# Kernel tuning notes

Measured on AMD Instinct MI355X. Metric: run time of the kernel, lower is better.

The kernel has to match this reference:

```python
import jax, jax.numpy as jnp
import numpy as np
import math

N_HEADS = 12
ROPE_DIM = 64
BASE = 10000.0


def _rope_tables(seq_len, dim):
    inv_freq = 1.0 / (BASE ** (jnp.arange(0, dim, 2, dtype=jnp.float32) / dim))
    t = jnp.arange(seq_len, dtype=jnp.float32)
    freqs = jnp.outer(t, inv_freq)                      # [S, dim/2]
    emb = jnp.concatenate([freqs, freqs], axis=-1)      # [S, dim]
    # broadcast shape [1, S, 1, dim]
    return jnp.cos(emb)[None, :, None, :], jnp.sin(emb)[None, :, None, :]


def _rotate_half(x):
    x1, x2 = jnp.split(x, 2, axis=-1)
    return jnp.concatenate([-x2, x1], axis=-1)


def setup_inputs() -> dict:
    key = jax.random.key(0)
    ks = jax.random.split(key, 9)
    B, S, E = 2, 2048, 768
    s = 1.0 / math.sqrt(E)
    return {
        "x": jax.random.normal(ks[0], (B, S, E), jnp.float32),
        "Wq": jax.random.normal(ks[1], (E, E), jnp.float32) * s,
        "bq": jax.random.normal(ks[2], (E,), jnp.float32) * 0.02,
        "Wk": jax.random.normal(ks[3], (E, E), jnp.float32) * s,
        "bk": jax.random.normal(ks[4], (E,), jnp.float32) * 0.02,
        "Wv": jax.random.normal(ks[5], (E, E), jnp.float32) * s,
        "bv": jax.random.normal(ks[6], (E,), jnp.float32) * 0.02,
        "Wp": jax.random.normal(ks[7], (E, E), jnp.float32) * s,
        "bp": jax.random.normal(ks[8], (E,), jnp.float32) * 0.02,
    }


def reference(x, Wq, bq, Wk, bk, Wv, bv, Wp, bp):
    B, S, E = x.shape
    H = N_HEADS
    D = E // H

    q = (x @ Wq + bq).reshape(B, S, H, D)
    k = (x @ Wk + bk).reshape(B, S, H, D)
    v = (x @ Wv + bv).reshape(B, S, H, D)

    # rotary on first ROPE_DIM dims (here ROPE_DIM == D, so full rotary)
    cos, sin = _rope_tables(S, ROPE_DIM)
    q_rot, q_pass = q[..., :ROPE_DIM], q[..., ROPE_DIM:]
    k_rot, k_pass = k[..., :ROPE_DIM], k[..., ROPE_DIM:]
    q_rot = q_rot * cos + _rotate_half(q_rot) * sin
    k_rot = k_rot * cos + _rotate_half(k_rot) * sin
    q = jnp.concatenate([q_rot, q_pass], axis=-1)
    k = jnp.concatenate([k_rot, k_pass], axis=-1)

    # scores [B, M, N, H]; mask before scaling (as in the torch code; -inf unchanged)
    att = jnp.einsum("bmhd,bnhd->bmnh", q, k)
    causal = jnp.tril(jnp.ones((S, S), dtype=bool))[None, :, :, None]
    att = jnp.where(causal, att, -jnp.inf)
    att = jax.nn.softmax(att / math.sqrt(D), axis=2)
    out = jnp.einsum("bmnh,bnhd->bmhd", att, v)

    return out.reshape(B, S, E) @ Wp + bp
```

## Files before the change

### kernel.cpp

```cpp
#include <hip/hip_runtime.h>
#include <stdint.h>

#define S_LEN 2048
#define EMB   768
#define NH    12
#define DH    64
#define M_TOT 4096
#define WELEM 589824
#define QELEM 3145728

typedef float  floatx4 __attribute__((ext_vector_type(4)));
typedef __bf16 bf16x8  __attribute__((ext_vector_type(8)));
typedef __bf16 bf16x4  __attribute__((ext_vector_type(4)));
typedef unsigned short ushortx4 __attribute__((ext_vector_type(4)));

__device__ __forceinline__ unsigned short f2bf(float f) {
    union { float f; unsigned u; } v; v.f = f;
    unsigned u = v.u;
    unsigned r = (u + 0x7FFFu + ((u >> 16) & 1u)) >> 16;
    return (unsigned short)r;
}

__device__ __forceinline__ void gl_lds16(const void* g, void* l) {
    __builtin_amdgcn_global_load_lds(
        (__attribute__((address_space(1))) const void*)g,
        (__attribute__((address_space(3))) void*)l, 16, 0, 0);
}

__global__ void cvt_all_kernel(const float* __restrict__ x, unsigned short* __restrict__ xb,
                               const float* __restrict__ W0, const float* __restrict__ W1,
                               const float* __restrict__ W2, const float* __restrict__ W3,
                               unsigned short* __restrict__ WT_all) {
    __shared__ float t[64][65];
    const int blk = blockIdx.x;
    if (blk < 3072) {
        int i = (blk * 256 + threadIdx.x) * 4;
        float4 v = *(const float4*)(x + i);
        ushortx4 r = { f2bf(v.x), f2bf(v.y), f2bf(v.z), f2bf(v.w) };
        *(ushortx4*)(xb + i) = r;
        return;
    }
    const int tc = blk - 3072;
    const int z = tc / 144, rr0 = tc % 144;
    const float* W = (z == 0) ? W0 : (z == 1 ? W1 : (z == 2 ? W2 : W3));
    unsigned short* O = WT_all + (size_t)z * WELEM;
    const int k0 = (rr0 % 12) * 64, n0 = (rr0 / 12) * 64;
    const int c = threadIdx.x & 63, r4 = threadIdx.x >> 6;
#pragma unroll
    for (int rr = 0; rr < 64; rr += 4) {
        int r = rr + r4;
        t[r][c] = W[(size_t)(k0 + r) * EMB + n0 + c];
    }
    __syncthreads();
#pragma unroll
    for (int rr = 0; rr < 64; rr += 4) {
        int nn = rr + r4;
        O[(size_t)(n0 + nn) * EMB + k0 + c] = f2bf(t[c][nn]);
    }
}

static __device__ __forceinline__ void gemm_core_64x128(
    const unsigned short* __restrict__ A, const unsigned short* __restrict__ BT,
    int m0, int n0, int K, int tid, floatx4 (&acc)[2][4],
    unsigned short* Als, unsigned short* Bls)
{
    const int lane = tid & 63;
    const int c0 = lane & 15, quad = lane >> 4;
    const int wave = tid >> 6;
    const int wm = (wave >> 1) * 32, wn = (wave & 1) * 64;

    for (int k0 = 0; k0 < K; k0 += 64) {
        __syncthreads();
#pragma unroll
        for (int it = 0; it < 2; ++it) {
            int ch = it * 256 + tid;
            int row = ch >> 3, cc = (ch & 7) ^ (row & 7);
            gl_lds16(A + (size_t)(m0 + row) * K + k0 + cc * 8, Als + ch * 8);
        }
#pragma unroll
        for (int it = 0; it < 4; ++it) {
            int ch = it * 256 + tid;
            int row = ch >> 3, cc = (ch & 7) ^ (row & 7);
            gl_lds16(BT + (size_t)(n0 + row) * K + k0 + cc * 8, Bls + ch * 8);
        }
        __syncthreads();
        bf16x8 af[2][2], bfv[4][2];
#pragma unroll
        for (int ii = 0; ii < 2; ++ii) {
            int row = wm + 16 * ii + c0;
#pragma unroll
            for (int h = 0; h < 2; ++h)
                af[ii][h] = *(const bf16x8*)(Als + row * 64 + (((4 * h + quad) ^ (row & 7)) * 8));
        }
#pragma unroll
        for (int jj = 0; jj < 4; ++jj) {
            int row = wn + 16 * jj + c0;
#pragma unroll
            for (int h = 0; h < 2; ++h)
                bfv[jj][h] = *(const bf16x8*)(Bls + row * 64 + (((4 * h + quad) ^ (row & 7)) * 8));
        }
#pragma unroll
        for (int ii = 0; ii < 2; ++ii)
#pragma unroll
            for (int jj = 0; jj < 4; ++jj) {
                acc[ii][jj] = __builtin_amdgcn_mfma_f32_16x16x32_bf16(af[ii][0], bfv[jj][0], acc[ii][jj], 0, 0, 0);
                acc[ii][jj] = __builtin_amdgcn_mfma_f32_16x16x32_bf16(af[ii][1], bfv[jj][1], acc[ii][jj], 0, 0, 0);
            }
    }
}

__global__ __launch_bounds__(256, 4) void qkv_kernel(
    const unsigned short* __restrict__ xb, const unsigned short* __restrict__ WT_all,
    const float* __restrict__ bq, const float* __restrict__ bk, const float* __restrict__ bv,
    unsigned short* __restrict__ qkv_out)
{
    __shared__ __align__(16) unsigned short Als[64 * 64];
    __shared__ __align__(16) unsigned short Bls[128 * 64];
    const int my = blockIdx.y;
    const int z = my / 6, n0 = (my % 6) * 128;
    const float* bias = (z == 0) ? bq : (z == 1 ? bk : bv);
    __bf16* Cout = (__bf16*)(qkv_out + (size_t)z * QELEM);
    const int m0 = blockIdx.x * 64;
    const int tid = threadIdx.x, lane = tid & 63, c0 = lane & 15, quad = lane >> 4, wave = tid >> 6;
    const int wm = (wave >> 1) * 32, wn = (wave & 1) * 64;

    floatx4 acc[2][4] = {};
    gemm_core_64x128(xb, WT_all + (size_t)z * WELEM, m0, n0, EMB, tid, acc, Als, Bls);

#pragma unroll
    for (int ii = 0; ii < 2; ++ii) {
#pragma unroll
        for (int r = 0; r < 4; ++r) {
            int m = m0 + wm + 16 * ii + quad * 4 + r;
            int b = m >> 11, s = m & (S_LEN - 1);
            float vals[4];
#pragma unroll
            for (int jj = 0; jj < 4; ++jj) vals[jj] = acc[ii][jj][r] + bias[n0 + wn + 16 * jj + c0];
            if (z < 2) {
#pragma unroll
                for (int jj = 0; jj < 2; ++jj) {
                    int d = 16 * jj + c0;
                    float f = exp2f((float)d * -0.41524101186092034f);
                    float th = (float)s * f;
                    float sn, cs; sincosf(th, &sn, &cs);
                    float lo = vals[jj], hi = vals[jj + 2];
                    vals[jj]     = lo * cs - hi * sn;
                    vals[jj + 2] = hi * cs + lo * sn;
                }
            }
            if (z == 0) {
#pragma unroll
                for (int jj = 0; jj < 4; ++jj) vals[jj] *= 0.18033688011112042f;
            }
#pragma unroll
            for (int jj = 0; jj < 4; ++jj) {
                int n = n0 + wn + 16 * jj + c0;
                int h = n >> 6, d = n & 63;
                if (z < 2)
                    Cout[((size_t)(b * NH + h) * S_LEN + s) * DH + d] = (__bf16)vals[jj];
                else
                    Cout[((size_t)(b * NH + h) * DH + d) * S_LEN + s] = (__bf16)vals[jj];
            }
        }
    }
}

__global__ __launch_bounds__(256, 3) void flash_kernel(
    const unsigned short* __restrict__ Qg, const unsigned short* __restrict__ Kg,
    const unsigned short* __restrict__ Vt, unsigned short* __restrict__ Og)
{
    __shared__ __align__(16) unsigned short Kls[2][64 * 64];
    __shared__ __align__(16) unsigned short Vls[2][64 * 64];
    __shared__ __align__(16) unsigned short Pls[4][32 * 72];

    const int blk = blockIdx.x;
    const int qt = 15 - (blk / 24);
    const int bh = blk % 24;
    const int b = bh / NH, h = bh % NH;
    const int m0 = qt * 128;
    const int tid = threadIdx.x, lane = tid & 63, wave = tid >> 6;
    const int c0 = lane & 15, quad = lane >> 4;
    const size_t gbase = (size_t)bh * S_LEN * DH;
    const int mrow0 = m0 + wave * 32 + c0;
    const int mrow1 = mrow0 + 16;

    bf16x8 qf[2][2];
    qf[0][0] = *(const bf16x8*)(Qg + gbase + (size_t)mrow0 * DH + quad * 8);
    qf[0][1] = *(const bf16x8*)(Qg + gbase + (size_t)mrow0 * DH + 32 + quad * 8);
    qf[1][0] = *(const bf16x8*)(Qg + gbase + (size_t)mrow1 * DH + quad * 8);
    qf[1][1] = *(const bf16x8*)(Qg + gbase + (size_t)mrow1 * DH + 32 + quad * 8);

    floatx4 oa[2][4] = {};
    float l_lane[2] = { 0.f, 0.f };
    const float C = 23.083120654223414f;
    const int ntiles = 2 * qt + 2;

#pragma unroll
    for (int it = 0; it < 2; ++it) {
        int ch = it * 256 + tid;
        int row = ch >> 3, cc = (ch & 7) ^ (row & 7);
        gl_lds16(Kg + gbase + (size_t)row * DH + cc * 8, &Kls[0][ch * 8]);
        gl_lds16(Vt + gbase + (size_t)row * S_LEN + cc * 8, &Vls[0][ch * 8]);
    }

    for (int nt = 0; nt < ntiles; ++nt) {
        __syncthreads();
        if (nt + 1 < ntiles) {
            int n0 = (nt + 1) * 64, buf = (nt + 1) & 1;
#pragma unroll
            for (int it = 0; it < 2; ++it) {
                int ch = it * 256 + tid;
                int row = ch >> 3, cc = (ch & 7) ^ (row & 7);
                gl_lds16(Kg + gbase + (size_t)(n0 + row) * DH + cc * 8, &Kls[buf][ch * 8]);
                gl_lds16(Vt + gbase + (size_t)row * S_LEN + n0 + cc * 8, &Vls[buf][ch * 8]);
            }
        }
        const unsigned short* Kb = Kls[nt & 1];
        const unsigned short* Vb = Vls[nt & 1];

        floatx4 sa[2][4];
        const floatx4 zz = { 0.f, 0.f, 0.f, 0.f };
#pragma unroll
        for (int jj = 0; jj < 4; ++jj) {
            int row = 16 * jj + c0;
            bf16x8 k0 = *(const bf16x8*)(Kb + row * 64 + ((quad ^ (row & 7)) * 8));
            bf16x8 k1 = *(const bf16x8*)(Kb + row * 64 + (((4 + quad) ^ (row & 7)) * 8));
#pragma unroll
            for (int s = 0; s < 2; ++s) {
                sa[s][jj] = __builtin_amdgcn_mfma_f32_16x16x32_bf16(k0, qf[s][0], zz, 0, 0, 0);
                sa[s][jj] = __builtin_amdgcn_mfma_f32_16x16x32_bf16(k1, qf[s][1], sa[s][jj], 0, 0, 0);
            }
        }
        if (nt >= ntiles - 2) {
            int nb0 = nt * 64 + quad * 4;
#pragma unroll
            for (int s = 0; s < 2; ++s) {
                int mr = mrow0 + s * 16;
#pragma unroll
                for (int jj = 0; jj < 4; ++jj)
#pragma unroll
                    for (int rr = 0; rr < 4; ++rr)
                        if (nb0 + 16 * jj + rr > mr) sa[s][jj][rr] = -1e30f;
            }
        }
#pragma unroll
        for (int s = 0; s < 2; ++s)
#pragma unroll
            for (int jj = 0; jj < 4; ++jj) {
                bf16x4 pw;
#pragma unroll
                for (int rr = 0; rr < 4; ++rr) {
                    float p = __builtin_amdgcn_exp2f(sa[s][jj][rr] - C);
                    l_lane[s] += p;
                    pw[rr] = (__bf16)p;
                }
                *(bf16x4*)(&Pls[wave][(s * 16 + c0) * 72 + 16 * jj + quad * 4]) = pw;
            }
#pragma unroll
        for (int h2 = 0; h2 < 2; ++h2) {
            bf16x8 pf0 = *(const bf16x8*)(&Pls[wave][c0 * 72 + 32 * h2 + quad * 8]);
            bf16x8 pf1 = *(const bf16x8*)(&Pls[wave][(16 + c0) * 72 + 32 * h2 + quad * 8]);
#pragma unroll
            for (int dt = 0; dt < 4; ++dt) {
                int row = 16 * dt + c0;
                bf16x8 vf = *(const bf16x8*)(Vb + row * 64 + (((4 * h2 + quad) ^ (row & 7)) * 8));
                oa[0][dt] = __builtin_amdgcn_mfma_f32_16x16x32_bf16(vf, pf0, oa[0][dt], 0, 0, 0);
                oa[1][dt] = __builtin_amdgcn_mfma_f32_16x16x32_bf16(vf, pf1, oa[1][dt], 0, 0, 0);
            }
        }
    }

    __bf16* Ob16 = (__bf16*)Og;
#pragma unroll
    for (int s = 0; s < 2; ++s) {
        float l = l_lane[s];
        l += __shfl_xor(l, 16, 64);
        l += __shfl_xor(l, 32, 64);
        const float rl = 1.0f / l;
        const int mr = mrow0 + s * 16;
#pragma unroll
        for (int dt = 0; dt < 4; ++dt) {
            bf16x4 ov;
#pragma unroll
            for (int rr = 0; rr < 4; ++rr) ov[rr] = (__bf16)(oa[s][dt][rr] * rl);
            *(bf16x4*)(Ob16 + ((size_t)(b * S_LEN + mr)) * EMB + h * DH + dt * 16 + quad * 4) = ov;
        }
    }
}

__global__ __launch_bounds__(256, 4) void proj_kernel(
    const unsigned short* __restrict__ Ob, const unsigned short* __restrict__ WpT,
    const float* __restrict__ bp, float* __restrict__ out)
{
    __shared__ __align__(16) unsigned short Als[64 * 64];
    __shared__ __align__(16) unsigned short Bls[128 * 64];
    const int m0 = blockIdx.x * 64, n0 = blockIdx.y * 128;
    const int tid = threadIdx.x, lane = tid & 63, c0 = lane & 15, quad = lane >> 4, wave = tid >> 6;
    const int wm = (wave >> 1) * 32, wn = (wave & 1) * 64;

    floatx4 acc[2][4] = {};
    gemm_core_64x128(Ob, WpT, m0, n0, EMB, tid, acc, Als, Bls);

#pragma unroll
    for (int ii = 0; ii < 2; ++ii)
#pragma unroll
        for (int r = 0; r < 4; ++r) {
            int m = m0 + wm + 16 * ii + quad * 4 + r;
#pragma unroll
            for (int jj = 0; jj < 4; ++jj) {
                int n = n0 + wn + 16 * jj + c0;
                out[(size_t)m * EMB + n] = acc[ii][jj][r] + bp[n];
            }
        }
}

extern "C" void kernel_launch(void* const* d_in, const int* in_sizes, int n_in,
                              void* d_out, int out_size, void* d_ws, size_t ws_size,
                              hipStream_t stream)
{
    (void)in_sizes; (void)n_in; (void)out_size;
    const float* x  = (const float*)d_in[0];
    const float* Wq = (const float*)d_in[1];
    const float* bq = (const float*)d_in[2];
    const float* Wk = (const float*)d_in[3];
    const float* bk = (const float*)d_in[4];
    const float* Wv = (const float*)d_in[5];
    const float* bv = (const float*)d_in[6];
    const float* Wp = (const float*)d_in[7];
    const float* bp = (const float*)d_in[8];

    unsigned short* ws  = (unsigned short*)d_ws;
    unsigned short* xb  = ws;
    unsigned short* WT  = xb + (size_t)QELEM;
    unsigned short* QKV = WT + 4 * (size_t)WELEM;
    unsigned short* Ob  = QKV + 3 * (size_t)QELEM;
    if (ws_size < ((size_t)QELEM * 5 + 4 * (size_t)WELEM) * 2) return;

    cvt_all_kernel<<<3648, 256, 0, stream>>>(x, xb, Wq, Wk, Wv, Wp, WT);
    qkv_kernel<<<dim3(64, 18), 256, 0, stream>>>(xb, WT, bq, bk, bv, QKV);
    flash_kernel<<<dim3(384), 256, 0, stream>>>(QKV, QKV + QELEM, QKV + 2 * (size_t)QELEM, Ob);
    proj_kernel<<<dim3(64, 6), 256, 0, stream>>>(Ob, WT + 3 * (size_t)WELEM, bp, (float*)d_out);
}
```

Before: 166.0 us.

## Triple-buffer LDS loads with single barrier and remap flash block order

Replaces the two-barrier load/compute loop in the GEMM core and the flash attention kernel with a three-stage ring of LDS buffers. The next tile is issued before compute, and partial vmcnt waits let one tile stay in flight behind a single s_barrier per iteration. It also permutes the flash block index so the heaviest causal query tiles are distributed differently across the launch. The larger LDS footprint lowers the launch-bounds occupancy target to 2, and the hand-written waitcnt counts must match the number of issued loads.

```diff
diff --git a/kernel.cpp b/kernel.cpp
--- a/kernel.cpp
+++ b/kernel.cpp
@@ -13,6 +13,9 @@
 typedef __bf16 bf16x8  __attribute__((ext_vector_type(8)));
 typedef __bf16 bf16x4  __attribute__((ext_vector_type(4)));
 typedef unsigned short ushortx4 __attribute__((ext_vector_type(4)));
+
+#define WAITVM(N)  __asm__ __volatile__("s_waitcnt vmcnt(" #N ")" ::: "memory")
+#define BARRIER()  __asm__ __volatile__("s_barrier" ::: "memory")
 
 __device__ __forceinline__ unsigned short f2bf(float f) {
     union { float f; unsigned u; } v; v.f = f;
@@ -68,36 +71,51 @@
     const int c0 = lane & 15, quad = lane >> 4;
     const int wave = tid >> 6;
     const int wm = (wave >> 1) * 32, wn = (wave & 1) * 64;
-
-    for (int k0 = 0; k0 < K; k0 += 64) {
-        __syncthreads();
-#pragma unroll
-        for (int it = 0; it < 2; ++it) {
-            int ch = it * 256 + tid;
-            int row = ch >> 3, cc = (ch & 7) ^ (row & 7);
-            gl_lds16(A + (size_t)(m0 + row) * K + k0 + cc * 8, Als + ch * 8);
-        }
-#pragma unroll
-        for (int it = 0; it < 4; ++it) {
-            int ch = it * 256 + tid;
-            int row = ch >> 3, cc = (ch & 7) ^ (row & 7);
-            gl_lds16(BT + (size_t)(n0 + row) * K + k0 + cc * 8, Bls + ch * 8);
-        }
-        __syncthreads();
+    const int nk = K / 64;
+
+    const int ar = tid >> 3, ac = (tid & 7);
+    const int br = tid >> 3, bc = (tid & 7);
+
+#define GEMM_STAGE(buf, kk)  do {                                              \
+        unsigned short* Ad = Als + (buf) * (64 * 64);                          \
+        unsigned short* Bd = Bls + (buf) * (128 * 64);                         \
+        _Pragma("unroll")                                                      \
+        for (int it = 0; it < 2; ++it) {                                       \
+            int row = ar + it * 32, cc = ac ^ (row & 7);                       \
+            gl_lds16(A + (size_t)(m0 + row) * K + (kk) + cc * 8,               \
+                     Ad + row * 64 + (ac ^ (row & 7)) * 8);                    \
+        }                                                                      \
+        _Pragma("unroll")                                                      \
+        for (int it = 0; it < 4; ++it) {                                       \
+            int row = br + it * 32, cc = bc ^ (row & 7);                       \
+            gl_lds16(BT + (size_t)(n0 + row) * K + (kk) + cc * 8,              \
+                     Bd + row * 64 + (bc ^ (row & 7)) * 8);                    \
+        }                                                                      \
+    } while (0)
+
+    GEMM_STAGE(0, 0);
+    int cur = 0;
+    for (int kt = 0; kt < nk; ++kt) {
+        int nxt = (cur == 2) ? 0 : cur + 1;
+        if (kt + 1 < nk) { GEMM_STAGE(nxt, (kt + 1) * 64); WAITVM(6); }
+        else             { WAITVM(0); }
+        BARRIER();
+        const unsigned short* Ab = Als + cur * (64 * 64);
+        const unsigned short* Bb = Bls + cur * (128 * 64);
         bf16x8 af[2][2], bfv[4][2];
 #pragma unroll
         for (int ii = 0; ii < 2; ++ii) {
             int row = wm + 16 * ii + c0;
 #pragma unroll
             for (int h = 0; h < 2; ++h)
-                af[ii][h] = *(const bf16x8*)(Als + row * 64 + (((4 * h + quad) ^ (row & 7)) * 8));
+                af[ii][h] = *(const bf16x8*)(Ab + row * 64 + (((4 * h + quad) ^ (row & 7)) * 8));
         }
 #pragma unroll
         for (int jj = 0; jj < 4; ++jj) {
             int row = wn + 16 * jj + c0;
 #pragma unroll
             for (int h = 0; h < 2; ++h)
-                bfv[jj][h] = *(const bf16x8*)(Bls + row * 64 + (((4 * h + quad) ^ (row & 7)) * 8));
+                bfv[jj][h] = *(const bf16x8*)(Bb + row * 64 + (((4 * h + quad) ^ (row & 7)) * 8));
         }
 #pragma unroll
         for (int ii = 0; ii < 2; ++ii)
@@ -106,16 +124,18 @@
                 acc[ii][jj] = __builtin_amdgcn_mfma_f32_16x16x32_bf16(af[ii][0], bfv[jj][0], acc[ii][jj], 0, 0, 0);
                 acc[ii][jj] = __builtin_amdgcn_mfma_f32_16x16x32_bf16(af[ii][1], bfv[jj][1], acc[ii][jj], 0, 0, 0);
             }
-    }
-}
-
-__global__ __launch_bounds__(256, 4) void qkv_kernel(
+        cur = nxt;
+    }
+#undef GEMM_STAGE
+}
+
+__global__ __launch_bounds__(256, 2) void qkv_kernel(
     const unsigned short* __restrict__ xb, const unsigned short* __restrict__ WT_all,
     const float* __restrict__ bq, const float* __restrict__ bk, const float* __restrict__ bv,
     unsigned short* __restrict__ qkv_out)
 {
-    __shared__ __align__(16) unsigned short Als[64 * 64];
-    __shared__ __align__(16) unsigned short Bls[128 * 64];
+    __shared__ __align__(16) unsigned short Als[3 * 64 * 64];
+    __shared__ __align__(16) unsigned short Bls[3 * 128 * 64];
     const int my = blockIdx.y;
     const int z = my / 6, n0 = (my % 6) * 128;
     const float* bias = (z == 0) ? bq : (z == 1 ? bk : bv);
@@ -165,17 +185,21 @@
     }
 }
 
-__global__ __launch_bounds__(256, 3) void flash_kernel(
+__global__ __launch_bounds__(256, 2) void flash_kernel(
     const unsigned short* __restrict__ Qg, const unsigned short* __restrict__ Kg,
     const unsigned short* __restrict__ Vt, unsigned short* __restrict__ Og)
 {
-    __shared__ __align__(16) unsigned short Kls[2][64 * 64];
-    __shared__ __align__(16) unsigned short Vls[2][64 * 64];
+    __shared__ __align__(16) unsigned short Kls[3][64 * 64];
+    __shared__ __align__(16) unsigned short Vls[3][64 * 64];
     __shared__ __align__(16) unsigned short Pls[4][32 * 72];
 
     const int blk = blockIdx.x;
-    const int qt = 15 - (blk / 24);
-    const int bh = blk % 24;
+    int R;
+    if (blk >= 128 && blk < 256) R = blk - 128;
+    else if (blk < 128)          R = 128 + blk;
+    else                         R = 639 - blk;
+    const int qt = 15 - (R / 24);
+    const int bh = R % 24;
     const int b = bh / NH, h = bh % NH;
     const int m0 = qt * 128;
     const int tid = threadIdx.x, lane = tid & 63, wave = tid >> 6;
@@ -195,28 +219,28 @@
     const float C = 23.083120654223414f;
     const int ntiles = 2 * qt + 2;
 
-#pragma unroll
-    for (int it = 0; it < 2; ++it) {
-        int ch = it * 256 + tid;
-        int row = ch >> 3, cc = (ch & 7) ^ (row & 7);
-        gl_lds16(Kg + gbase + (size_t)row * DH + cc * 8, &Kls[0][ch * 8]);
-        gl_lds16(Vt + gbase + (size_t)row * S_LEN + cc * 8, &Vls[0][ch * 8]);
-    }
-
+    const int srow = tid >> 3, sc = tid & 7;
+
+#define FLASH_STAGE(buf, n0s)  do {                                            \
+        _Pragma("unroll")                                                      \
+        for (int it = 0; it < 2; ++it) {                                       \
+            int row = srow + it * 32, cc = sc ^ (row & 7);                     \
+            gl_lds16(Kg + gbase + (size_t)((n0s) + row) * DH + cc * 8,         \
+                     &Kls[buf][row * 64 + cc * 8]);                            \
+            gl_lds16(Vt + gbase + (size_t)row * S_LEN + (n0s) + cc * 8,        \
+                     &Vls[buf][row * 64 + cc * 8]);                            \
+        }                                                                      \
+    } while (0)
+
+    FLASH_STAGE(0, 0);
+    int cur = 0;
     for (int nt = 0; nt < ntiles; ++nt) {
-        __syncthreads();
-        if (nt + 1 < ntiles) {
-            int n0 = (nt + 1) * 64, buf = (nt + 1) & 1;
-#pragma unroll
-            for (int it = 0; it < 2; ++it) {
-                int ch = it * 256 + tid;
-                int row = ch >> 3, cc = (ch & 7) ^ (row & 7);
-                gl_lds16(Kg + gbase + (size_t)(n0 + row) * DH + cc * 8, &Kls[buf][ch * 8]);
-                gl_lds16(Vt + gbase + (size_t)row * S_LEN + n0 + cc * 8, &Vls[buf][ch * 8]);
-            }
-        }
-        const unsigned short* Kb = Kls[nt & 1];
-        const unsigned short* Vb = Vls[nt & 1];
+        int nxt = (cur == 2) ? 0 : cur + 1;
+        if (nt + 1 < ntiles) { FLASH_STAGE(nxt, (nt + 1) * 64); WAITVM(4); }
+        else                 { WAITVM(0); }
+        BARRIER();
+        const unsigned short* Kb = Kls[cur];
+        const unsigned short* Vb = Vls[cur];
 
         floatx4 sa[2][4];
         const floatx4 zz = { 0.f, 0.f, 0.f, 0.f };
@@ -268,7 +292,9 @@
                 oa[1][dt] = __builtin_amdgcn_mfma_f32_16x16x32_bf16(vf, pf1, oa[1][dt], 0, 0, 0);
             }
         }
-    }
+        cur = nxt;
+    }
+#undef FLASH_STAGE
 
     __bf16* Ob16 = (__bf16*)Og;
 #pragma unroll
@@ -288,12 +314,12 @@
     }
 }
 
-__global__ __launch_bounds__(256, 4) void proj_kernel(
+__global__ __launch_bounds__(256, 2) void proj_kernel(
     const unsigned short* __restrict__ Ob, const unsigned short* __restrict__ WpT,
     const float* __restrict__ bp, float* __restrict__ out)
 {
-    __shared__ __align__(16) unsigned short Als[64 * 64];
-    __shared__ __align__(16) unsigned short Bls[128 * 64];
+    __shared__ __align__(16) unsigned short Als[3 * 64 * 64];
+    __shared__ __align__(16) unsigned short Bls[3 * 128 * 64];
     const int m0 = blockIdx.x * 64, n0 = blockIdx.y * 128;
     const int tid = threadIdx.x, lane = tid & 63, c0 = lane & 15, quad = lane >> 4, wave = tid >> 6;
     const int wm = (wave >> 1) * 32, wn = (wave & 1) * 64;
```

Result: no change. 167.1 us (+0.6%).
